# Kernel tuning notes

Hardware: AMD Instinct MI355X
Metric: run time of the kernel (lower is better)

Reference implementation:

```python
import jax, jax.numpy as jnp
import numpy as np

N, T, D = 64, 2048, 512
NEG = -1e9


def setup_inputs() -> dict:
    key = jax.random.key(0)
    k1, k2, k3, k4 = jax.random.split(key, 4)
    return {
        "query": jax.random.normal(k1, (N, D), dtype=jnp.float32),
        "key": jax.random.normal(k2, (T, N, D), dtype=jnp.float32),
        "value": jax.random.normal(k3, (T, N, D), dtype=jnp.float32),
        "lens": jax.random.randint(k4, (N,), 0, T, dtype=jnp.int64)
        if jax.config.jax_enable_x64 else jax.random.randint(k4, (N,), 0, T, dtype=jnp.int32),
    }


def reference(query, key, value, lens):
    # key/value: (T, N, D) -> (N, T, D)
    k = jnp.transpose(key, (1, 0, 2))
    v = jnp.transpose(value, (1, 0, 2))
    # energy: (N, T) = per-batch matvec key @ query
    energy = jnp.einsum('ntd,nd->nt', k, query)
    # length mask: positions >= lens are masked with -1e9 (as in masked_fill_)
    mask = jnp.arange(energy.shape[1])[None, :] >= lens[:, None]
    energy = jnp.where(mask, jnp.asarray(NEG, energy.dtype), energy)
    attention = jax.nn.softmax(energy, axis=1)
    # context: (N, D)
    context = jnp.einsum('nt,ntd->nd', attention, v)
    return context
```

## Files before the change

kernel.cpp:

```cpp
#include <hip/hip_runtime.h>
#include <math.h>

#define N_B 64
#define T_LEN 2048
#define D_DIM 512
#define NEG (-1e9f)
#define G_BLK 1792
#define MIN_W 16
#define J_MAX 132


__device__ __forceinline__ float dot8(const float4& qa, const float4& qb,
                                      const float4& ka, const float4& kb) {
    return qa.x * ka.x + qa.y * ka.y + qa.z * ka.z + qa.w * ka.w
         + qb.x * kb.x + qb.y * kb.y + qb.z * kb.z + qb.w * kb.w;
}

__device__ __forceinline__ int useful_rows(int len) {
    return (len == 0) ? T_LEN : len;
}

__global__ __launch_bounds__(256) void attn_partial(
    const float* __restrict__ q,
    const float* __restrict__ key,
    const float* __restrict__ val,
    const int*   __restrict__ lens,
    float* __restrict__ m_ws,
    float* __restrict__ l_ws,
    float* __restrict__ o_ws)
{
    const int tid  = threadIdx.x;
    const int wave = tid >> 6;
    const int lane = tid & 63;
    const int d0   = 2 * tid;
    const size_t rstride = (size_t)N_B * D_DIM;

    __shared__ int   pre_sm[N_B + 1];
    __shared__ float acc_sm[4][D_DIM];
    __shared__ float ml_sm[4][2];

    if (wave == 0) {
        int incl = useful_rows(lens[lane]);
        #pragma unroll
        for (int off = 1; off < 64; off <<= 1) {
            const int y = __shfl_up(incl, off);
            if (lane >= off) incl += y;
        }
        if (lane == 0) pre_sm[0] = 0;
        pre_sm[1 + lane] = incl;
    }
    __syncthreads();

    const int total = pre_sm[N_B];
    int W = (total + G_BLK - 1) / G_BLK;
    if (W < MIN_W) W = MIN_W;
    const int r0 = blockIdx.x * W;
    if (r0 >= total) return;
    const int r1 = min(r0 + W, total);

    int lo = 0, hi = N_B;
    while (hi - lo > 1) {
        const int mid = (lo + hi) >> 1;
        if (pre_sm[mid] <= r0) lo = mid; else hi = mid;
    }
    int n = lo;
    int r = r0;

    while (r < r1) {
        const int sn    = pre_sm[n];
        const int sn1   = pre_sm[n + 1];
        const int ta    = r - sn;
        const int tb    = min(r1, sn1) - sn;
        const int j     = blockIdx.x - (sn / W);
        const int len_n = lens[n];

        float acc[8];
        #pragma unroll
        for (int jj = 0; jj < 8; ++jj) acc[jj] = 0.0f;
        float m = -INFINITY, l = 0.0f;

        if (len_n == 0) {
            int cnt = 0;
            const float* vr = val + ((size_t)(ta + wave) * N_B + n) * D_DIM
                            + 8 * lane;
            for (int t = ta + wave; t < tb; t += 4) {
                const float4 va = *reinterpret_cast<const float4*>(vr);
                const float4 vb = *reinterpret_cast<const float4*>(vr + 4);
                vr += 4 * rstride;
                acc[0] += va.x; acc[1] += va.y; acc[2] += va.z; acc[3] += va.w;
                acc[4] += vb.x; acc[5] += vb.y; acc[6] += vb.z; acc[7] += vb.w;
                ++cnt;
            }
            m = NEG;
            l = (float)cnt;
        } else {
            int t = ta + wave;
            if (t < tb) {
                const float4* q4 = reinterpret_cast<const float4*>(
                    q + (size_t)n * D_DIM) + 2 * lane;
                const float4 qa = q4[0];
                const float4 qb = q4[1];

                const float* kr = key + ((size_t)t * N_B + n) * D_DIM + 8 * lane;
                const float* vr = val + ((size_t)t * N_B + n) * D_DIM + 8 * lane;

                float4 ka = *reinterpret_cast<const float4*>(kr);
                float4 kb = *reinterpret_cast<const float4*>(kr + 4);
                float4 na = ka, nb = kb;

                for (; t < tb; t += 4) {
                    const float4 va = *reinterpret_cast<const float4*>(vr);
                    const float4 vb = *reinterpret_cast<const float4*>(vr + 4);
                    vr += 4 * rstride;
                    if (t + 4 < tb) {
                        na = *reinterpret_cast<const float4*>(kr + 4 * rstride);
                        nb = *reinterpret_cast<const float4*>(kr + 4 * rstride + 4);
                    }
                    kr += 4 * rstride;

                    float e = dot8(qa, qb, ka, kb);
                    #pragma unroll
                    for (int off = 32; off; off >>= 1) e += __shfl_xor(e, off);

                    if (e > m) {
                        const float sc = __expf(m - e);
                        l *= sc;
                        #pragma unroll
                        for (int jj = 0; jj < 8; ++jj) acc[jj] *= sc;
                        m = e;
                    }
                    const float p = __expf(e - m);
                    l += p;
                    acc[0] += p * va.x; acc[1] += p * va.y;
                    acc[2] += p * va.z; acc[3] += p * va.w;
                    acc[4] += p * vb.x; acc[5] += p * vb.y;
                    acc[6] += p * vb.z; acc[7] += p * vb.w;

                    ka = na; kb = nb;
                }
            }
        }

        *reinterpret_cast<float4*>(&acc_sm[wave][8 * lane]) =
            make_float4(acc[0], acc[1], acc[2], acc[3]);
        *reinterpret_cast<float4*>(&acc_sm[wave][8 * lane + 4]) =
            make_float4(acc[4], acc[5], acc[6], acc[7]);
        if (lane == 0) { ml_sm[wave][0] = m; ml_sm[wave][1] = l; }
        __syncthreads();

        const float m0 = ml_sm[0][0], m1 = ml_sm[1][0];
        const float m2 = ml_sm[2][0], m3 = ml_sm[3][0];
        const float M  = fmaxf(fmaxf(m0, m1), fmaxf(m2, m3));
        const float s0 = __expf(m0 - M), s1 = __expf(m1 - M);
        const float s2 = __expf(m2 - M), s3 = __expf(m3 - M);

        float2 rr;
        rr.x = s0 * acc_sm[0][d0]     + s1 * acc_sm[1][d0]
             + s2 * acc_sm[2][d0]     + s3 * acc_sm[3][d0];
        rr.y = s0 * acc_sm[0][d0 + 1] + s1 * acc_sm[1][d0 + 1]
             + s2 * acc_sm[2][d0 + 1] + s3 * acc_sm[3][d0 + 1];
        *reinterpret_cast<float2*>(
            o_ws + ((size_t)n * J_MAX + j) * D_DIM + d0) = rr;

        if (tid == 0) {
            m_ws[n * J_MAX + j] = M;
            l_ws[n * J_MAX + j] = s0 * ml_sm[0][1] + s1 * ml_sm[1][1]
                                + s2 * ml_sm[2][1] + s3 * ml_sm[3][1];
        }

        r = min(r1, sn1);
        ++n;
        if (r < r1) __syncthreads();
    }
}

__global__ __launch_bounds__(256) void attn_combine(
    const int*   __restrict__ lens,
    const float* __restrict__ m_ws,
    const float* __restrict__ l_ws,
    const float* __restrict__ o_ws,
    float* __restrict__ out)
{
    const int n   = blockIdx.x;
    const int tid = threadIdx.x;

    __shared__ float s_sm[J_MAX];
    __shared__ float S_sm;
    __shared__ int   J_sm;

    if (tid < 64) {
        int incl = useful_rows(lens[tid]);
        #pragma unroll
        for (int off = 1; off < 64; off <<= 1) {
            const int y = __shfl_up(incl, off);
            if (tid >= off) incl += y;
        }
        const int total = __shfl(incl, 63);
        int W = (total + G_BLK - 1) / G_BLK;
        if (W < MIN_W) W = MIN_W;
        const int sn1 = __shfl(incl, n);
        const int sn  = (n == 0) ? 0 : __shfl(incl, n - 1);
        const int b0  = sn / W;
        const int b1  = (sn1 - 1) / W;
        const int J   = b1 - b0 + 1;
        if (tid == 0) J_sm = J;

        float mj[3], lj[3];
        float M = -INFINITY;
        #pragma unroll
        for (int k = 0; k < 3; ++k) {
            const int jdx = tid + 64 * k;
            const bool ok = (jdx < J);
            mj[k] = ok ? m_ws[n * J_MAX + jdx] : -INFINITY;
            lj[k] = ok ? l_ws[n * J_MAX + jdx] : 0.0f;
            M = fmaxf(M, mj[k]);
        }
        #pragma unroll
        for (int off = 32; off; off >>= 1) M = fmaxf(M, __shfl_xor(M, off));
        float S = 0.0f;
        #pragma unroll
        for (int k = 0; k < 3; ++k) {
            const int jdx = tid + 64 * k;
            const float s = __expf(mj[k] - M);
            if (jdx < J) s_sm[jdx] = s;
            S += s * lj[k];
        }
        #pragma unroll
        for (int off = 32; off; off >>= 1) S += __shfl_xor(S, off);
        if (tid == 0) S_sm = S;
    }
    __syncthreads();

    const int J = J_sm;
    const float inv = 1.0f / S_sm;
    const int d = blockIdx.y * 256 + tid;
    const float* op = o_ws + (size_t)n * J_MAX * D_DIM + d;

    float a0 = 0, a1 = 0, a2 = 0, a3 = 0, a4 = 0, a5 = 0, a6 = 0, a7 = 0;
    int jj = 0;
    for (; jj + 7 < J; jj += 8) {
        a0 += s_sm[jj]     * op[(size_t)jj * D_DIM];
        a1 += s_sm[jj + 1] * op[(size_t)(jj + 1) * D_DIM];
        a2 += s_sm[jj + 2] * op[(size_t)(jj + 2) * D_DIM];
        a3 += s_sm[jj + 3] * op[(size_t)(jj + 3) * D_DIM];
        a4 += s_sm[jj + 4] * op[(size_t)(jj + 4) * D_DIM];
        a5 += s_sm[jj + 5] * op[(size_t)(jj + 5) * D_DIM];
        a6 += s_sm[jj + 6] * op[(size_t)(jj + 6) * D_DIM];
        a7 += s_sm[jj + 7] * op[(size_t)(jj + 7) * D_DIM];
    }
    for (; jj < J; ++jj)
        a0 += s_sm[jj] * op[(size_t)jj * D_DIM];

    out[(size_t)n * D_DIM + d] =
        (((a0 + a1) + (a2 + a3)) + ((a4 + a5) + (a6 + a7))) * inv;
}

extern "C" void kernel_launch(void* const* d_in, const int* in_sizes, int n_in,
                              void* d_out, int out_size, void* d_ws, size_t ws_size,
                              hipStream_t stream) {
    const float* q    = (const float*)d_in[0];
    const float* key  = (const float*)d_in[1];
    const float* val  = (const float*)d_in[2];
    const int*   lens = (const int*)d_in[3];
    float*       out  = (float*)d_out;

    float* m_ws = (float*)d_ws;
    float* l_ws = m_ws + N_B * J_MAX;
    float* o_ws = l_ws + N_B * J_MAX;

    attn_partial<<<G_BLK, 256, 0, stream>>>(q, key, val, lens,
                                            m_ws, l_ws, o_ws);
    attn_combine<<<dim3(N_B, D_DIM / 256), 256, 0, stream>>>(lens, m_ws, l_ws,
                                                             o_ws, out);
}
```

Baseline: 55.09 us.

## Fuse partial and combine kernels via cooperative launch with grid sync

Merges the split-T partial attention kernel and the combine kernel into one cooperative kernel, separated by a grid-wide sync. The grid size now comes from an occupancy query and is capped at the previous block count, with the per-block row count W derived from gridDim. The aim is to drop a second kernel launch and the recomputation of the lengths prefix sum. In exchange it pays for a grid barrier, and the grid may shrink if occupancy is lower, which gives each block more rows.

```diff
diff --git a/kernel.cpp b/kernel.cpp
--- a/kernel.cpp
+++ b/kernel.cpp
@@ -1,11 +1,14 @@
 #include <hip/hip_runtime.h>
+#include <hip/hip_cooperative_groups.h>
 #include <math.h>
+
+namespace cg = cooperative_groups;
 
 #define N_B 64
 #define T_LEN 2048
 #define D_DIM 512
 #define NEG (-1e9f)
-#define G_BLK 1792
+#define G_MAX 1792
 #define MIN_W 16
 #define J_MAX 132
 
@@ -20,14 +23,15 @@
     return (len == 0) ? T_LEN : len;
 }
 
-__global__ __launch_bounds__(256) void attn_partial(
+__global__ __launch_bounds__(256) void attn_fused(
     const float* __restrict__ q,
     const float* __restrict__ key,
     const float* __restrict__ val,
     const int*   __restrict__ lens,
     float* __restrict__ m_ws,
     float* __restrict__ l_ws,
-    float* __restrict__ o_ws)
+    float* __restrict__ o_ws,
+    float* __restrict__ out)
 {
     const int tid  = threadIdx.x;
     const int wave = tid >> 6;
@@ -52,157 +56,145 @@
     __syncthreads();
 
     const int total = pre_sm[N_B];
-    int W = (total + G_BLK - 1) / G_BLK;
+    int W = (total + (int)gridDim.x - 1) / (int)gridDim.x;
     if (W < MIN_W) W = MIN_W;
     const int r0 = blockIdx.x * W;
-    if (r0 >= total) return;
-    const int r1 = min(r0 + W, total);
-
-    int lo = 0, hi = N_B;
-    while (hi - lo > 1) {
-        const int mid = (lo + hi) >> 1;
-        if (pre_sm[mid] <= r0) lo = mid; else hi = mid;
-    }
-    int n = lo;
-    int r = r0;
-
-    while (r < r1) {
-        const int sn    = pre_sm[n];
-        const int sn1   = pre_sm[n + 1];
-        const int ta    = r - sn;
-        const int tb    = min(r1, sn1) - sn;
-        const int j     = blockIdx.x - (sn / W);
-        const int len_n = lens[n];
-
-        float acc[8];
-        #pragma unroll
-        for (int jj = 0; jj < 8; ++jj) acc[jj] = 0.0f;
-        float m = -INFINITY, l = 0.0f;
-
-        if (len_n == 0) {
-            int cnt = 0;
-            const float* vr = val + ((size_t)(ta + wave) * N_B + n) * D_DIM
-                            + 8 * lane;
-            for (int t = ta + wave; t < tb; t += 4) {
-                const float4 va = *reinterpret_cast<const float4*>(vr);
-                const float4 vb = *reinterpret_cast<const float4*>(vr + 4);
-                vr += 4 * rstride;
-                acc[0] += va.x; acc[1] += va.y; acc[2] += va.z; acc[3] += va.w;
-                acc[4] += vb.x; acc[5] += vb.y; acc[6] += vb.z; acc[7] += vb.w;
-                ++cnt;
-            }
-            m = NEG;
-            l = (float)cnt;
-        } else {
-            int t = ta + wave;
-            if (t < tb) {
-                const float4* q4 = reinterpret_cast<const float4*>(
-                    q + (size_t)n * D_DIM) + 2 * lane;
-                const float4 qa = q4[0];
-                const float4 qb = q4[1];
-
-                const float* kr = key + ((size_t)t * N_B + n) * D_DIM + 8 * lane;
-                const float* vr = val + ((size_t)t * N_B + n) * D_DIM + 8 * lane;
-
-                float4 ka = *reinterpret_cast<const float4*>(kr);
-                float4 kb = *reinterpret_cast<const float4*>(kr + 4);
-                float4 na = ka, nb = kb;
-
-                for (; t < tb; t += 4) {
+
+    if (r0 < total) {
+        const int r1 = min(r0 + W, total);
+
+        int lo = 0, hi = N_B;
+        while (hi - lo > 1) {
+            const int mid = (lo + hi) >> 1;
+            if (pre_sm[mid] <= r0) lo = mid; else hi = mid;
+        }
+        int n = lo;
+        int r = r0;
+
+        while (r < r1) {
+            const int sn    = pre_sm[n];
+            const int sn1   = pre_sm[n + 1];
+            const int ta    = r - sn;
+            const int tb    = min(r1, sn1) - sn;
+            const int j     = blockIdx.x - (sn / W);
+            const int len_n = lens[n];
+
+            float acc[8];
+            #pragma unroll
+            for (int jj = 0; jj < 8; ++jj) acc[jj] = 0.0f;
+            float m = -INFINITY, l = 0.0f;
+
+            if (len_n == 0) {
+                int cnt = 0;
+                const float* vr = val + ((size_t)(ta + wave) * N_B + n) * D_DIM
+                                + 8 * lane;
+                for (int t = ta + wave; t < tb; t += 4) {
                     const float4 va = *reinterpret_cast<const float4*>(vr);
                     const float4 vb = *reinterpret_cast<const float4*>(vr + 4);
                     vr += 4 * rstride;
-                    if (t + 4 < tb) {
-                        na = *reinterpret_cast<const float4*>(kr + 4 * rstride);
-                        nb = *reinterpret_cast<const float4*>(kr + 4 * rstride + 4);
+                    acc[0] += va.x; acc[1] += va.y; acc[2] += va.z; acc[3] += va.w;
+                    acc[4] += vb.x; acc[5] += vb.y; acc[6] += vb.z; acc[7] += vb.w;
+                    ++cnt;
+                }
+                m = NEG;
+                l = (float)cnt;
+            } else {
+                int t = ta + wave;
+                if (t < tb) {
+                    const float4* q4 = reinterpret_cast<const float4*>(
+                        q + (size_t)n * D_DIM) + 2 * lane;
+                    const float4 qa = q4[0];
+                    const float4 qb = q4[1];
+
+                    const float* kr = key + ((size_t)t * N_B + n) * D_DIM + 8 * lane;
+                    const float* vr = val + ((size_t)t * N_B + n) * D_DIM + 8 * lane;
+
+                    float4 ka = *reinterpret_cast<const float4*>(kr);
+                    float4 kb = *reinterpret_cast<const float4*>(kr + 4);
+                    float4 na = ka, nb = kb;
+
+                    for (; t < tb; t += 4) {
+                        const float4 va = *reinterpret_cast<const float4*>(vr);
+                        const float4 vb = *reinterpret_cast<const float4*>(vr + 4);
+                        vr += 4 * rstride;
+                        if (t + 4 < tb) {
+                            na = *reinterpret_cast<const float4*>(kr + 4 * rstride);
+                            nb = *reinterpret_cast<const float4*>(kr + 4 * rstride + 4);
+                        }
+                        kr += 4 * rstride;
+
+                        float e = dot8(qa, qb, ka, kb);
+                        #pragma unroll
+                        for (int off = 32; off; off >>= 1) e += __shfl_xor(e, off);
+
+                        if (e > m) {
+                            const float sc = __expf(m - e);
+                            l *= sc;
+                            #pragma unroll
+                            for (int jj = 0; jj < 8; ++jj) acc[jj] *= sc;
+                            m = e;
+                        }
+                        const float p = __expf(e - m);
+                        l += p;
+                        acc[0] += p * va.x; acc[1] += p * va.y;
+                        acc[2] += p * va.z; acc[3] += p * va.w;
+                        acc[4] += p * vb.x; acc[5] += p * vb.y;
+                        acc[6] += p * vb.z; acc[7] += p * vb.w;
+
+                        ka = na; kb = nb;
                     }
-                    kr += 4 * rstride;
-
-                    float e = dot8(qa, qb, ka, kb);
-                    #pragma unroll
-                    for (int off = 32; off; off >>= 1) e += __shfl_xor(e, off);
-
-                    if (e > m) {
-                        const float sc = __expf(m - e);
-                        l *= sc;
-                        #pragma unroll
-                        for (int jj = 0; jj < 8; ++jj) acc[jj] *= sc;
-                        m = e;
-                    }
-                    const float p = __expf(e - m);
-                    l += p;
-                    acc[0] += p * va.x; acc[1] += p * va.y;
-                    acc[2] += p * va.z; acc[3] += p * va.w;
-                    acc[4] += p * vb.x; acc[5] += p * vb.y;
-                    acc[6] += p * vb.z; acc[7] += p * vb.w;
-
-                    ka = na; kb = nb;
                 }
             }
-        }
-
-        *reinterpret_cast<float4*>(&acc_sm[wave][8 * lane]) =
-            make_float4(acc[0], acc[1], acc[2], acc[3]);
-        *reinterpret_cast<float4*>(&acc_sm[wave][8 * lane + 4]) =
-            make_float4(acc[4], acc[5], acc[6], acc[7]);
-        if (lane == 0) { ml_sm[wave][0] = m; ml_sm[wave][1] = l; }
-        __syncthreads();
-
-        const float m0 = ml_sm[0][0], m1 = ml_sm[1][0];
-        const float m2 = ml_sm[2][0], m3 = ml_sm[3][0];
-        const float M  = fmaxf(fmaxf(m0, m1), fmaxf(m2, m3));
-        const float s0 = __expf(m0 - M), s1 = __expf(m1 - M);
-        const float s2 = __expf(m2 - M), s3 = __expf(m3 - M);
-
-        float2 rr;
-        rr.x = s0 * acc_sm[0][d0]     + s1 * acc_sm[1][d0]
-             + s2 * acc_sm[2][d0]     + s3 * acc_sm[3][d0];
-        rr.y = s0 * acc_sm[0][d0 + 1] + s1 * acc_sm[1][d0 + 1]
-             + s2 * acc_sm[2][d0 + 1] + s3 * acc_sm[3][d0 + 1];
-        *reinterpret_cast<float2*>(
-            o_ws + ((size_t)n * J_MAX + j) * D_DIM + d0) = rr;
-
-        if (tid == 0) {
-            m_ws[n * J_MAX + j] = M;
-            l_ws[n * J_MAX + j] = s0 * ml_sm[0][1] + s1 * ml_sm[1][1]
-                                + s2 * ml_sm[2][1] + s3 * ml_sm[3][1];
-        }
-
-        r = min(r1, sn1);
-        ++n;
-        if (r < r1) __syncthreads();
-    }
-}
-
-__global__ __launch_bounds__(256) void attn_combine(
-    const int*   __restrict__ lens,
-    const float* __restrict__ m_ws,
-    const float* __restrict__ l_ws,
-    const float* __restrict__ o_ws,
-    float* __restrict__ out)
-{
-    const int n   = blockIdx.x;
-    const int tid = threadIdx.x;
+
+            *reinterpret_cast<float4*>(&acc_sm[wave][8 * lane]) =
+                make_float4(acc[0], acc[1], acc[2], acc[3]);
+            *reinterpret_cast<float4*>(&acc_sm[wave][8 * lane + 4]) =
+                make_float4(acc[4], acc[5], acc[6], acc[7]);
+            if (lane == 0) { ml_sm[wave][0] = m; ml_sm[wave][1] = l; }
+            __syncthreads();
+
+            const float m0 = ml_sm[0][0], m1 = ml_sm[1][0];
+            const float m2 = ml_sm[2][0], m3 = ml_sm[3][0];
+            const float M  = fmaxf(fmaxf(m0, m1), fmaxf(m2, m3));
+            const float s0 = __expf(m0 - M), s1 = __expf(m1 - M);
+            const float s2 = __expf(m2 - M), s3 = __expf(m3 - M);
+
+            float2 rr;
+            rr.x = s0 * acc_sm[0][d0]     + s1 * acc_sm[1][d0]
+                 + s2 * acc_sm[2][d0]     + s3 * acc_sm[3][d0];
+            rr.y = s0 * acc_sm[0][d0 + 1] + s1 * acc_sm[1][d0 + 1]
+                 + s2 * acc_sm[2][d0 + 1] + s3 * acc_sm[3][d0 + 1];
+            *reinterpret_cast<float2*>(
+                o_ws + ((size_t)n * J_MAX + j) * D_DIM + d0) = rr;
+
+            if (tid == 0) {
+                m_ws[n * J_MAX + j] = M;
+                l_ws[n * J_MAX + j] = s0 * ml_sm[0][1] + s1 * ml_sm[1][1]
+                                    + s2 * ml_sm[2][1] + s3 * ml_sm[3][1];
+            }
+
+            r = min(r1, sn1);
+            ++n;
+            if (r < r1) __syncthreads();
+        }
+    }
+
+    cg::this_grid().sync();
+
+    if (blockIdx.x >= 2 * N_B) return;
+    const int n = blockIdx.x >> 1;
+    const int h = blockIdx.x & 1;
 
     __shared__ float s_sm[J_MAX];
     __shared__ float S_sm;
     __shared__ int   J_sm;
 
     if (tid < 64) {
-        int incl = useful_rows(lens[tid]);
-        #pragma unroll
-        for (int off = 1; off < 64; off <<= 1) {
-            const int y = __shfl_up(incl, off);
-            if (tid >= off) incl += y;
-        }
-        const int total = __shfl(incl, 63);
-        int W = (total + G_BLK - 1) / G_BLK;
-        if (W < MIN_W) W = MIN_W;
-        const int sn1 = __shfl(incl, n);
-        const int sn  = (n == 0) ? 0 : __shfl(incl, n - 1);
-        const int b0  = sn / W;
-        const int b1  = (sn1 - 1) / W;
-        const int J   = b1 - b0 + 1;
+        const int sn1x = pre_sm[1 + n];
+        const int snx  = pre_sm[n];
+        const int b0   = snx / W;
+        const int b1   = (sn1x - 1) / W;
+        const int J    = b1 - b0 + 1;
         if (tid == 0) J_sm = J;
 
         float mj[3], lj[3];
@@ -233,7 +225,7 @@
 
     const int J = J_sm;
     const float inv = 1.0f / S_sm;
-    const int d = blockIdx.y * 256 + tid;
+    const int d = h * 256 + tid;
     const float* op = o_ws + (size_t)n * J_MAX * D_DIM + d;
 
     float a0 = 0, a1 = 0, a2 = 0, a3 = 0, a4 = 0, a5 = 0, a6 = 0, a7 = 0;
@@ -268,8 +260,16 @@
     float* l_ws = m_ws + N_B * J_MAX;
     float* o_ws = l_ws + N_B * J_MAX;
 
-    attn_partial<<<G_BLK, 256, 0, stream>>>(q, key, val, lens,
-                                            m_ws, l_ws, o_ws);
-    attn_combine<<<dim3(N_B, D_DIM / 256), 256, 0, stream>>>(lens, m_ws, l_ws,
-                                                             o_ws, out);
-}
+    int occ = 0;
+    hipOccupancyMaxActiveBlocksPerMultiprocessor(&occ, (const void*)attn_fused,
+                                                 256, 0);
+    if (occ < 1) occ = 1;
+    int grid = occ * 256;
+    if (grid > G_MAX) grid = G_MAX;
+    if (grid < 2 * N_B) grid = 2 * N_B;
+
+    void* args[] = {(void*)&q, (void*)&key, (void*)&val, (void*)&lens,
+                    (void*)&m_ws, (void*)&l_ws, (void*)&o_ws, (void*)&out};
+    hipLaunchCooperativeKernel((const void*)attn_fused, dim3(grid), dim3(256),
+                               args, 0, stream);
+}
```

Measured after the change: 131.8 us. 139% more time.
